# Optimization experiments

Hardware: AMD Instinct MI355X
Metric: run time of the kernel (lower is better)

Reference implementation:

```python
import jax, jax.numpy as jnp
import numpy as np
import math

B, L, D, H = 4, 2048, 1024, 16
HD = D // H


def setup_inputs() -> dict:
    key = jax.random.key(0)
    k1, k2, k3 = jax.random.split(key, 3)
    x = jax.random.normal(k1, (B, L, D), dtype=jnp.float32)
    # Linear weights stored as [in, out] so y = x @ W (equivalent to torch x @ W.T)
    Wqkv = jax.random.normal(k2, (D, 3 * D), dtype=jnp.float32) * (1.0 / math.sqrt(D))
    Wproj = jax.random.normal(k3, (D, D), dtype=jnp.float32) * (1.0 / math.sqrt(D))
    attn_mask = jnp.tril(jnp.ones((L, L), dtype=bool))  # True = attend (causal)
    key_padding_mask = jnp.zeros((B, L), dtype=bool)     # True = padded (none here)
    return {"x": x, "Wqkv": Wqkv, "Wproj": Wproj,
            "attn_mask": attn_mask, "key_padding_mask": key_padding_mask}


def reference(x, Wqkv, Wproj, attn_mask, key_padding_mask):
    Bx, Lx, Dx = x.shape
    qkv = x @ Wqkv                              # [B, L, 3D]
    q, k, v = jnp.split(qkv, 3, axis=-1)
    def shape(t):
        return t.reshape(Bx, Lx, H, HD).transpose(0, 2, 1, 3)  # [B, H, L, hd]
    q, k, v = shape(q), shape(k), shape(v)
    att = jnp.einsum('bhqd,bhkd->bhqk', q, k) / math.sqrt(HD)  # [B, H, L, L]
    neg_inf = jnp.float32(-jnp.inf)
    att = jnp.where(attn_mask[None, None, :, :], att, neg_inf)
    att = jnp.where(key_padding_mask[:, None, None, :], neg_inf, att)
    att = jax.nn.softmax(att, axis=-1)
    y = jnp.einsum('bhqk,bhkd->bhqd', att, v)   # [B, H, L, hd]
    y = y.transpose(0, 2, 1, 3).reshape(Bx, Lx, Dx)
    return y @ Wproj
```

## Files before the change

kernel.cpp:

```cpp
#include <hip/hip_runtime.h>
#include <cstdint>
#include <cstddef>


typedef __attribute__((ext_vector_type(8))) __bf16 bf16x8;
typedef __attribute__((ext_vector_type(4))) __bf16 bf16x4;
typedef __attribute__((ext_vector_type(4))) float f32x4;

__device__ __forceinline__ f32x4 mfma_bf16(bf16x8 a, bf16x8 b, f32x4 c) {
  return __builtin_amdgcn_mfma_f32_16x16x32_bf16(a, b, c, 0, 0, 0);
}

__device__ __forceinline__ void async_copy16(const void* gsrc, void* ldsdst) {
  __builtin_amdgcn_global_load_lds(
      (const __attribute__((address_space(1))) void*)gsrc,
      (__attribute__((address_space(3))) void*)ldsdst, 16, 0, 0);
}

__global__ __launch_bounds__(256) void f32_to_bf16(
    const float* __restrict__ in, __bf16* __restrict__ out) {
  const size_t i = ((size_t)blockIdx.x * 256 + threadIdx.x) * 4;
  const float4 v = *(const float4*)&in[i];
  bf16x4 o = {(__bf16)v.x, (__bf16)v.y, (__bf16)v.z, (__bf16)v.w};
  *(bf16x4*)&out[i] = o;
}

__global__ __launch_bounds__(256) void transpose_f32_bf16(
    const float* __restrict__ in, __bf16* __restrict__ out, int R, int C) {
  __shared__ float tile[32][33];
  const int c0 = blockIdx.x * 32;
  const int r0 = blockIdx.y * 32;
  const int tx = threadIdx.x & 31;
  const int ty = threadIdx.x >> 5;
#pragma unroll
  for (int i = 0; i < 32; i += 8)
    tile[ty + i][tx] = in[(size_t)(r0 + ty + i) * C + c0 + tx];
  __syncthreads();
#pragma unroll
  for (int i = 0; i < 32; i += 8)
    out[(size_t)(c0 + ty + i) * R + r0 + tx] = (__bf16)tile[tx][ty + i];
}


__global__ __launch_bounds__(256) void gemm_bt_f32out(
    const __bf16* __restrict__ A, const __bf16* __restrict__ BT,
    float* __restrict__ C, int M, int N, int K) {
  __shared__ __bf16 As[128 * 32];
  __shared__ __bf16 Bs[128 * 32];
  const int tid = threadIdx.x;
  const int wave = tid >> 6;
  const int lane = tid & 63;
  const int n16 = lane & 15;
  const int quad = lane >> 4;
  const int m0 = blockIdx.x * 128;
  const int n0 = blockIdx.y * 128;
  const int wr = wave >> 1;
  const int wc = wave & 1;

  const f32x4 zero = {0.f, 0.f, 0.f, 0.f};
  f32x4 acc[4][4];
#pragma unroll
  for (int i = 0; i < 4; ++i)
#pragma unroll
    for (int j = 0; j < 4; ++j) acc[i][j] = zero;

  const int KT = K >> 5;
  for (int kt = 0; kt < KT; ++kt) {
    const int k0 = kt << 5;
#pragma unroll
    for (int r = 0; r < 2; ++r) {
      const int li = (r << 8) + tid;
      const int row = li >> 2;
      const int kp8 = (li & 3) << 3;
      const int lbase = ((r << 8) + (wave << 6)) << 3;
      async_copy16(&A[(size_t)(m0 + row) * K + k0 + kp8], &As[lbase]);
      async_copy16(&BT[(size_t)(n0 + row) * K + k0 + kp8], &Bs[lbase]);
    }
    __syncthreads();
    bf16x8 af[4], bf[4];
#pragma unroll
    for (int t = 0; t < 4; ++t) {
      af[t] = *(const bf16x8*)&As[(wr * 64 + t * 16 + n16) * 32 + quad * 8];
      bf[t] = *(const bf16x8*)&Bs[(wc * 64 + t * 16 + n16) * 32 + quad * 8];
    }
#pragma unroll
    for (int mt = 0; mt < 4; ++mt)
#pragma unroll
      for (int nt = 0; nt < 4; ++nt)
        acc[mt][nt] = mfma_bf16(af[mt], bf[nt], acc[mt][nt]);
    __syncthreads();
  }
#pragma unroll
  for (int mt = 0; mt < 4; ++mt) {
#pragma unroll
    for (int r = 0; r < 4; ++r) {
      const int m = m0 + wr * 64 + mt * 16 + quad * 4 + r;
#pragma unroll
      for (int nt = 0; nt < 4; ++nt) {
        const int n = n0 + wc * 64 + nt * 16 + n16;
        C[(size_t)m * N + n] = acc[mt][nt][r];
      }
    }
  }
}

__global__ __launch_bounds__(256) void gemm_qkv(
    const __bf16* __restrict__ A, const __bf16* __restrict__ BT,
    __bf16* __restrict__ Q, __bf16* __restrict__ Kh, __bf16* __restrict__ VT) {
  __shared__ __bf16 As[128 * 32];
  __shared__ __bf16 Bs[128 * 32];
  const int tid = threadIdx.x;
  const int wave = tid >> 6;
  const int lane = tid & 63;
  const int n16 = lane & 15;
  const int quad = lane >> 4;
  const int m0 = blockIdx.x * 128;
  const int n0 = blockIdx.y * 128;
  const int wr = wave >> 1;
  const int wc = wave & 1;
  const int K = 1024;

  const f32x4 zero = {0.f, 0.f, 0.f, 0.f};
  f32x4 acc[4][4];
#pragma unroll
  for (int i = 0; i < 4; ++i)
#pragma unroll
    for (int j = 0; j < 4; ++j) acc[i][j] = zero;

  for (int kt = 0; kt < 32; ++kt) {
    const int k0 = kt << 5;
#pragma unroll
    for (int r = 0; r < 2; ++r) {
      const int li = (r << 8) + tid;
      const int row = li >> 2;
      const int kp8 = (li & 3) << 3;
      const int lbase = ((r << 8) + (wave << 6)) << 3;
      async_copy16(&A[(size_t)(m0 + row) * K + k0 + kp8], &As[lbase]);
      async_copy16(&BT[(size_t)(n0 + row) * K + k0 + kp8], &Bs[lbase]);
    }
    __syncthreads();
    bf16x8 af[4], bf[4];
#pragma unroll
    for (int t = 0; t < 4; ++t) {
      af[t] = *(const bf16x8*)&As[(wr * 64 + t * 16 + n16) * 32 + quad * 8];
      bf[t] = *(const bf16x8*)&Bs[(wc * 64 + t * 16 + n16) * 32 + quad * 8];
    }
#pragma unroll
    for (int mt = 0; mt < 4; ++mt)
#pragma unroll
      for (int nt = 0; nt < 4; ++nt)
        acc[mt][nt] = mfma_bf16(af[mt], bf[nt], acc[mt][nt]);
    __syncthreads();
  }

  __syncthreads();
  const int b = m0 >> 11;
  __bf16* tw = (wave < 2 ? As : Bs) + (wave & 1) * 2048;
  const int l0w = (m0 & 2047) + wr * 64;

  if (n0 < 2048) {
    const float QSCALE = 0.125f * 1.44269504089f;
    const bool isQ = (n0 < 1024);
    const int h = ((n0 & 1023) >> 6) + wc;
    __bf16* dst = isQ ? Q : Kh;
    const size_t base = ((size_t)(b * 16 + h) * 2048) * 64;
#pragma unroll
    for (int pass = 0; pass < 2; ++pass) {
#pragma unroll
      for (int mt = 2 * pass; mt < 2 * pass + 2; ++mt) {
#pragma unroll
        for (int nt = 0; nt < 4; ++nt)
#pragma unroll
          for (int r = 0; r < 4; ++r) {
            const int hd = nt * 16 + n16;
            const int mm = (mt & 1) * 16 + quad * 4 + r;
            const float v =
                isQ ? acc[mt][nt][r] * QSCALE : acc[mt][nt][r];
            tw[mm * 64 + (((hd >> 3) ^ (mm & 7)) << 3) + (hd & 7)] =
                (__bf16)v;
          }
      }
#pragma unroll
      for (int i = 0; i < 4; ++i) {
        const int c = lane + 64 * i;
        const int row = c >> 3;
        const int hd0 = (c & 7) << 3;
        const int phys = (c & 7) ^ (row & 7);
        const bf16x8 v = *(const bf16x8*)&tw[row * 64 + phys * 8];
        *(bf16x8*)&dst[base + (size_t)(l0w + pass * 32 + row) * 64 + hd0] = v;
      }
    }
  } else {
    const int h = ((n0 - 2048) >> 6) + wc;
    const size_t bhead = (size_t)(b * 16 + h);
#pragma unroll
    for (int pass = 0; pass < 2; ++pass) {
#pragma unroll
      for (int nt = 2 * pass; nt < 2 * pass + 2; ++nt) {
#pragma unroll
        for (int mt = 0; mt < 4; ++mt)
#pragma unroll
          for (int r = 0; r < 4; ++r) {
            const int hdp = (nt & 1) * 16 + n16;
            const int mm = mt * 16 + quad * 4 + r;
            const int phys = (mm >> 3) ^ (hdp & 7);
            tw[hdp * 64 + phys * 8 + (mm & 7)] = (__bf16)acc[mt][nt][r];
          }
      }
#pragma unroll
      for (int i = 0; i < 4; ++i) {
        const int c = lane + 64 * i;
        const int row = c >> 3;
        const int phys = (c & 7) ^ (row & 7);
        const bf16x8 v = *(const bf16x8*)&tw[row * 64 + phys * 8];
        *(bf16x8*)&VT[(bhead * 64 + pass * 32 + row) * 2048 + l0w +
                      (c & 7) * 8] = v;
      }
    }
  }
}

__global__ __launch_bounds__(256, 4) void flash_attn(
    const __bf16* __restrict__ Q, const __bf16* __restrict__ Kh,
    const __bf16* __restrict__ VT, __bf16* __restrict__ Y) {
  __shared__ __bf16 KsB[2][32 * 64];
  __shared__ __bf16 VsB[2][64 * 32];
  __shared__ __bf16 Ps[4][16 * 40];
  const int bh = blockIdx.x;
  const int p = blockIdx.y;
  const int tid = threadIdx.x;
  const int wave = tid >> 6;
  const int lane = tid & 63;
  const int n16 = lane & 15;
  const int quad = lane >> 4;
  __bf16* pb = Ps[wave];
  const __bf16* Qb = Q + (size_t)bh * 2048 * 64;
  const __bf16* Kb = Kh + (size_t)bh * 2048 * 64;
  const __bf16* Vb = VT + (size_t)bh * 64 * 2048;
  const int b = bh >> 4;
  const int h = bh & 15;
  const f32x4 zero = {0.f, 0.f, 0.f, 0.f};

  const int krow = wave * 8 + (lane >> 3);
  const int kcol8 = (((lane & 7) ^ (lane >> 3)) << 3);
  const int vrow = wave * 16 + (lane >> 2);
  const int vcol8 = (((lane & 3) ^ quad) << 3);

#pragma unroll
  for (int t = 0; t < 2; ++t) {
    const int qt = t == 0 ? p : 31 - p;
    const int q0w = qt * 64 + wave * 16;

    bf16x8 qf[2];
#pragma unroll
    for (int kh = 0; kh < 2; ++kh)
      qf[kh] = *(const bf16x8*)&Qb[(size_t)(q0w + n16) * 64 + kh * 32 +
                                   quad * 8];

    f32x4 o[4];
#pragma unroll
    for (int j = 0; j < 4; ++j) o[j] = zero;
    float lsum = 0.f;

    const int nsteps = 2 * qt + 2;

    async_copy16(&Kb[(size_t)krow * 64 + kcol8], &KsB[0][wave * 512]);
    async_copy16(&Vb[(size_t)vrow * 2048 + vcol8], &VsB[0][wave * 512]);

    for (int kt = 0; kt < nsteps; ++kt) {
      const int buf = kt & 1;
      const int c0 = kt * 32;
      __syncthreads();
      if (kt + 1 < nsteps) {
        const int nb = buf ^ 1;
        const int cn = c0 + 32;
        async_copy16(&Kb[(size_t)(cn + krow) * 64 + kcol8],
                     &KsB[nb][wave * 512]);
        async_copy16(&Vb[(size_t)vrow * 2048 + cn + vcol8],
                     &VsB[nb][wave * 512]);
      }
      const __bf16* ks = KsB[buf];
      const __bf16* vs = VsB[buf];

      f32x4 s[2];
      s[0] = zero;
      s[1] = zero;
#pragma unroll
      for (int ct = 0; ct < 2; ++ct) {
#pragma unroll
        for (int kh = 0; kh < 2; ++kh) {
          const bf16x8 kf = *(const bf16x8*)&ks[(ct * 16 + n16) * 64 +
                                                (((kh * 4 + quad) ^ (n16 & 7))
                                                 << 3)];
          s[ct] = mfma_bf16(kf, qf[kh], s[ct]);
        }
      }
      if (kt >= 2 * qt) {
        const int myq = q0w + n16;
#pragma unroll
        for (int ct = 0; ct < 2; ++ct)
#pragma unroll
          for (int r = 0; r < 4; ++r) {
            const int kcol = c0 + ct * 16 + quad * 4 + r;
            float e = __builtin_amdgcn_exp2f(s[ct][r]);
            e = (kcol <= myq) ? e : 0.f;
            s[ct][r] = e;
            lsum += e;
          }
      } else {
#pragma unroll
        for (int ct = 0; ct < 2; ++ct)
#pragma unroll
          for (int r = 0; r < 4; ++r) {
            const float e = __builtin_amdgcn_exp2f(s[ct][r]);
            s[ct][r] = e;
            lsum += e;
          }
      }
#pragma unroll
      for (int ct = 0; ct < 2; ++ct) {
        const bf16x4 pk = {(__bf16)s[ct][0], (__bf16)s[ct][1],
                           (__bf16)s[ct][2], (__bf16)s[ct][3]};
        *(bf16x4*)&pb[n16 * 40 + ct * 16 + quad * 4] = pk;
      }
      const bf16x8 pa = *(const bf16x8*)&pb[n16 * 40 + quad * 8];
#pragma unroll
      for (int ht = 0; ht < 4; ++ht) {
        const bf16x8 vf = *(const bf16x8*)&vs[(ht * 16 + n16) * 32 +
                                              ((quad ^ (n16 >> 2)) << 3)];
        o[ht] = mfma_bf16(pa, vf, o[ht]);
      }
    }

    lsum += __shfl_xor(lsum, 16);
    lsum += __shfl_xor(lsum, 32);
    const float inv = 1.0f / lsum;
#pragma unroll
    for (int r = 0; r < 4; ++r) {
      const float invr = __shfl(inv, quad * 4 + r);
      const int row = q0w + quad * 4 + r;
#pragma unroll
      for (int ht = 0; ht < 4; ++ht)
        Y[(size_t)(b * 2048 + row) * 1024 + h * 64 + ht * 16 + n16] =
            (__bf16)(o[ht][r] * invr);
    }
  }
}

extern "C" void kernel_launch(void* const* d_in, const int* in_sizes, int n_in,
                              void* d_out, int out_size, void* d_ws,
                              size_t ws_size, hipStream_t stream) {
  const float* x = (const float*)d_in[0];
  const float* Wqkv = (const float*)d_in[1];
  const float* Wproj = (const float*)d_in[2];
  float* out = (float*)d_out;

  char* ws = (char*)d_ws;
  __bf16* xb = (__bf16*)ws;     ws += (size_t)8192 * 1024 * 2;
  __bf16* WqkvT = (__bf16*)ws;  ws += (size_t)3072 * 1024 * 2;
  __bf16* WprojT = (__bf16*)ws; ws += (size_t)1024 * 1024 * 2;
  __bf16* Qs = (__bf16*)ws;     ws += (size_t)64 * 2048 * 64 * 2;
  __bf16* Ks = (__bf16*)ws;     ws += (size_t)64 * 2048 * 64 * 2;
  __bf16* VTs = (__bf16*)ws;    ws += (size_t)64 * 64 * 2048 * 2;
  __bf16* attn = xb;

  f32_to_bf16<<<8192, 256, 0, stream>>>(x, xb);
  transpose_f32_bf16<<<dim3(96, 32), 256, 0, stream>>>(Wqkv, WqkvT, 1024, 3072);
  transpose_f32_bf16<<<dim3(32, 32), 256, 0, stream>>>(Wproj, WprojT, 1024, 1024);
  gemm_qkv<<<dim3(64, 24), 256, 0, stream>>>(xb, WqkvT, Qs, Ks, VTs);
  flash_attn<<<dim3(64, 16), 256, 0, stream>>>(Qs, Ks, VTs, attn);
  gemm_bt_f32out<<<dim3(64, 8), 256, 0, stream>>>(attn, WprojT, out,
                                                  8192, 1024, 1024);
}
```

Baseline: 255.0 us.

## Triple-buffer flash-attention K/V loads and merge prep kernels into one launch

Flash attention moves from double to triple buffering of K/V tiles. The next two tiles are prefetched with async LDS copies, and each step waits with a partial vmcnt wait plus a raw s_barrier instead of __syncthreads, so more load latency overlaps with compute. Separately, the f32-to-bf16 conversion and the two weight transposes become a single prep kernel to cut launch overhead. The extra LDS buffer raises shared memory per block, which could lower occupancy. The hand-written waitcnt/barrier asm has to match the per-wave outstanding load count exactly.

```diff
diff --git a/kernel.cpp b/kernel.cpp
--- a/kernel.cpp
+++ b/kernel.cpp
@@ -17,19 +17,38 @@
       (__attribute__((address_space(3))) void*)ldsdst, 16, 0, 0);
 }
 
-__global__ __launch_bounds__(256) void f32_to_bf16(
-    const float* __restrict__ in, __bf16* __restrict__ out) {
-  const size_t i = ((size_t)blockIdx.x * 256 + threadIdx.x) * 4;
-  const float4 v = *(const float4*)&in[i];
-  bf16x4 o = {(__bf16)v.x, (__bf16)v.y, (__bf16)v.z, (__bf16)v.w};
-  *(bf16x4*)&out[i] = o;
-}
-
-__global__ __launch_bounds__(256) void transpose_f32_bf16(
-    const float* __restrict__ in, __bf16* __restrict__ out, int R, int C) {
+__device__ __forceinline__ void wait2_barrier() {
+  asm volatile("s_waitcnt vmcnt(2)\n\ts_barrier" ::: "memory");
+}
+__device__ __forceinline__ void wait0_barrier() {
+  asm volatile("s_waitcnt vmcnt(0)\n\ts_barrier" ::: "memory");
+}
+
+__global__ __launch_bounds__(256) void prep(
+    const float* __restrict__ x, __bf16* __restrict__ xb,
+    const float* __restrict__ Wq, __bf16* __restrict__ WqT,
+    const float* __restrict__ Wp, __bf16* __restrict__ WpT) {
+  const int bid = blockIdx.x;
+  if (bid < 8192) {
+    const size_t i = ((size_t)bid * 256 + threadIdx.x) * 4;
+    const float4 v = *(const float4*)&x[i];
+    bf16x4 o = {(__bf16)v.x, (__bf16)v.y, (__bf16)v.z, (__bf16)v.w};
+    *(bf16x4*)&xb[i] = o;
+    return;
+  }
   __shared__ float tile[32][33];
-  const int c0 = blockIdx.x * 32;
-  const int r0 = blockIdx.y * 32;
+  const float* in;
+  __bf16* out;
+  int C, t;
+  if (bid < 11264) {
+    t = bid - 8192;  in = Wq; out = WqT; C = 3072;
+  } else {
+    t = bid - 11264; in = Wp; out = WpT; C = 1024;
+  }
+  const int R = 1024;
+  const int tilesx = C >> 5;
+  const int c0 = (t % tilesx) * 32;
+  const int r0 = (t / tilesx) * 32;
   const int tx = threadIdx.x & 31;
   const int ty = threadIdx.x >> 5;
 #pragma unroll
@@ -174,10 +193,8 @@
           for (int r = 0; r < 4; ++r) {
             const int hd = nt * 16 + n16;
             const int mm = (mt & 1) * 16 + quad * 4 + r;
-            const float v =
-                isQ ? acc[mt][nt][r] * QSCALE : acc[mt][nt][r];
-            tw[mm * 64 + (((hd >> 3) ^ (mm & 7)) << 3) + (hd & 7)] =
-                (__bf16)v;
+            const float v = isQ ? acc[mt][nt][r] * QSCALE : acc[mt][nt][r];
+            tw[mm * 64 + (((hd >> 3) ^ (mm & 7)) << 3) + (hd & 7)] = (__bf16)v;
           }
       }
 #pragma unroll
@@ -223,8 +240,8 @@
 __global__ __launch_bounds__(256, 4) void flash_attn(
     const __bf16* __restrict__ Q, const __bf16* __restrict__ Kh,
     const __bf16* __restrict__ VT, __bf16* __restrict__ Y) {
-  __shared__ __bf16 KsB[2][32 * 64];
-  __shared__ __bf16 VsB[2][64 * 32];
+  __shared__ __bf16 KsB[3][32 * 64];
+  __shared__ __bf16 VsB[3][64 * 32];
   __shared__ __bf16 Ps[4][16 * 40];
   const int bh = blockIdx.x;
   const int p = blockIdx.y;
@@ -264,21 +281,27 @@
 
     const int nsteps = 2 * qt + 2;
 
+    __syncthreads();
     async_copy16(&Kb[(size_t)krow * 64 + kcol8], &KsB[0][wave * 512]);
     async_copy16(&Vb[(size_t)vrow * 2048 + vcol8], &VsB[0][wave * 512]);
+    async_copy16(&Kb[(size_t)(32 + krow) * 64 + kcol8], &KsB[1][wave * 512]);
+    async_copy16(&Vb[(size_t)vrow * 2048 + 32 + vcol8], &VsB[1][wave * 512]);
 
     for (int kt = 0; kt < nsteps; ++kt) {
-      const int buf = kt & 1;
-      const int c0 = kt * 32;
-      __syncthreads();
-      if (kt + 1 < nsteps) {
-        const int nb = buf ^ 1;
-        const int cn = c0 + 32;
+      if (kt + 1 < nsteps)
+        wait2_barrier();
+      else
+        wait0_barrier();
+      if (kt + 2 < nsteps) {
+        const int nb = (kt + 2) % 3;
+        const int cn = (kt + 2) * 32;
         async_copy16(&Kb[(size_t)(cn + krow) * 64 + kcol8],
                      &KsB[nb][wave * 512]);
         async_copy16(&Vb[(size_t)vrow * 2048 + cn + vcol8],
                      &VsB[nb][wave * 512]);
       }
+      const int buf = kt % 3;
+      const int c0 = kt * 32;
       const __bf16* ks = KsB[buf];
       const __bf16* vs = VsB[buf];
 
@@ -364,9 +387,7 @@
   __bf16* VTs = (__bf16*)ws;    ws += (size_t)64 * 64 * 2048 * 2;
   __bf16* attn = xb;
 
-  f32_to_bf16<<<8192, 256, 0, stream>>>(x, xb);
-  transpose_f32_bf16<<<dim3(96, 32), 256, 0, stream>>>(Wqkv, WqkvT, 1024, 3072);
-  transpose_f32_bf16<<<dim3(32, 32), 256, 0, stream>>>(Wproj, WprojT, 1024, 1024);
+  prep<<<12288, 256, 0, stream>>>(x, xb, Wqkv, WqkvT, Wproj, WprojT);
   gemm_qkv<<<dim3(64, 24), 256, 0, stream>>>(xb, WqkvT, Qs, Ks, VTs);
   flash_attn<<<dim3(64, 16), 256, 0, stream>>>(Qs, Ks, VTs, attn);
   gemm_bt_f32out<<<dim3(64, 8), 256, 0, stream>>>(attn, WprojT, out,
```

Measured after the change: 259.0 us. Within noise of the previous version (+1.5%).
